# Kernel optimization log

Hardware: AMD Instinct MI355X
Metric: run time of the kernel (lower is better)

## Reference

```python
import jax, jax.numpy as jnp
import numpy as np

N_AGENTS = 12
N_THREADS = 4096
DIM = 3
N_VEC = 4
HID = 64
INV_NF = 32
LAYERS = 2
N = N_THREADS * N_AGENTS


def _intra_graph_edges():
    # fully-connected directed edges within each env's agent graph
    i, j = np.meshgrid(np.arange(N_AGENTS), np.arange(N_AGENTS), indexing='ij')
    mask = i != j
    ri, ci = i[mask], j[mask]  # [132]
    off = (np.arange(N_THREADS) * N_AGENTS)[:, None]
    row = (ri[None, :] + off).reshape(-1).astype(np.int32)
    col = (ci[None, :] + off).reshape(-1).astype(np.int32)
    return jnp.asarray(row), jnp.asarray(col)


def setup_inputs() -> dict:
    key = jax.random.key(0)
    ks = jax.random.split(key, 16)
    s = 0.05
    row, col = _intra_graph_edges()
    return {
        'h0': jax.random.normal(ks[0], (N, INV_NF), jnp.float32),
        'x0': jax.random.normal(ks[1], (N, DIM, N_VEC), jnp.float32),
        'W_embed': jax.random.normal(ks[2], (INV_NF, HID), jnp.float32) * s,
        'b_embed': jnp.zeros((HID,), jnp.float32),
        'We1': jax.random.normal(ks[3], (LAYERS, 2 * HID + N_VEC, HID), jnp.float32) * s,
        'be1': jnp.zeros((LAYERS, HID), jnp.float32),
        'We2': jax.random.normal(ks[4], (LAYERS, HID, HID), jnp.float32) * s,
        'be2': jnp.zeros((LAYERS, HID), jnp.float32),
        'Wx': jax.random.normal(ks[5], (LAYERS, HID, N_VEC), jnp.float32) * s,
        'bx': jnp.zeros((LAYERS, N_VEC), jnp.float32),
        'Wh1': jax.random.normal(ks[6], (LAYERS, 2 * HID, HID), jnp.float32) * s,
        'bh1': jnp.zeros((LAYERS, HID), jnp.float32),
        'Wh2': jax.random.normal(ks[7], (LAYERS, HID, HID), jnp.float32) * s,
        'bh2': jnp.zeros((LAYERS, HID), jnp.float32),
        'w_act': jax.random.normal(ks[8], (N_VEC,), jnp.float32) * s,
        'log_std': jnp.full((DIM,), -0.5, jnp.float32),
        'row': row,
        'col': col,
    }


def reference(h0, x0, W_embed, b_embed, We1, be1, We2, be2, Wx, bx,
              Wh1, bh1, Wh2, bh2, w_act, log_std, row, col):
    silu = jax.nn.silu
    n = h0.shape[0]
    h = h0 @ W_embed + b_embed            # node embedding, [N, HID]
    x = x0                                 # equivariant features, [N, DIM, N_VEC]
    deg = jnp.maximum(jax.ops.segment_sum(jnp.ones_like(row, jnp.float32), row, num_segments=n), 1.0)
    for l in range(LAYERS):
        hi, hj = h[row], h[col]
        diff = x[row] - x[col]                        # [E, DIM, N_VEC]
        radial = jnp.sum(diff * diff, axis=1)          # [E, N_VEC]
        m = silu(jnp.concatenate([hi, hj, radial], -1) @ We1[l] + be1[l])
        m = silu(m @ We2[l] + be2[l])                  # edge messages [E, HID]
        wc = m @ Wx[l] + bx[l]                         # per-vector coord weights [E, N_VEC]
        x = x + jax.ops.segment_sum(diff * wc[:, None, :], row, num_segments=n) / deg[:, None, None]
        agg = jax.ops.segment_sum(m, row, num_segments=n)
        h = h + silu(jnp.concatenate([h, agg], -1) @ Wh1[l] + bh1[l]) @ Wh2[l] + bh2[l]
    mu = jnp.einsum('ndv,v->nd', x, w_act)             # act_net: Linear(N_VEC,1,bias=False)
    actions = mu                                        # deterministic: mode of Normal(mu, std)
    log_probs = jnp.broadcast_to(-log_std - 0.5 * jnp.log(2.0 * jnp.pi), mu.shape)
    actions = actions.reshape(N_THREADS, N_AGENTS, DIM)
    log_probs = log_probs.reshape(N_THREADS, N_AGENTS, DIM)
    return actions, log_probs
```

## Files before the change

### kernel.cpp

```cpp
#include <hip/hip_runtime.h>

#define NAG 12
#define NTH 4096
#define NEDGE 132
#define LDB 72
#define LDT 20

typedef __bf16 bf16_8 __attribute__((ext_vector_type(8)));
typedef __bf16 bf16_4 __attribute__((ext_vector_type(4)));
typedef float  f32x4  __attribute__((ext_vector_type(4)));

#define MFMA(a,b,c) __builtin_amdgcn_mfma_f32_16x16x32_bf16((a),(b),(c),0,0,0)

#define WS_FRAGS 100
#define WS_BIAS_F32 25600
#define WS_BX_F32   27648
#define WS_BYTES 111104

__device__ __forceinline__ float silu_f(float z) {
    float e = __expf(-z);
    return z * __builtin_amdgcn_rcpf(1.0f + e);
}

__device__ __forceinline__ bf16_8 loadB64(const float* __restrict__ W, int kbase, int n, int q) {
    bf16_8 b;
    #pragma unroll
    for (int j = 0; j < 8; ++j) b[j] = (__bf16)W[(kbase + q*8 + j) * 64 + n];
    return b;
}

__device__ __forceinline__ bf16_8 packA8(const float* S) {
    f32x4 u = *(const f32x4*)S, v = *(const f32x4*)(S + 4);
    bf16_8 a;
    a[0]=(__bf16)u.x; a[1]=(__bf16)u.y; a[2]=(__bf16)u.z; a[3]=(__bf16)u.w;
    a[4]=(__bf16)v.x; a[5]=(__bf16)v.y; a[6]=(__bf16)v.z; a[7]=(__bf16)v.w;
    return a;
}

__global__ __launch_bounds__(64) void prep_frags(
    const float* __restrict__ W_embed, const float* __restrict__ We1,
    const float* __restrict__ We2, const float* __restrict__ Wh1,
    const float* __restrict__ Wh2,
    const float* __restrict__ be1, const float* __restrict__ be2,
    const float* __restrict__ bh1, const float* __restrict__ bh2,
    const float* __restrict__ bx, __bf16* __restrict__ wsb)
{
    const int f = blockIdx.x, lane = threadIdx.x;
    const int q = lane >> 4, n16 = lane & 15;
    float* wsf = (float*)wsb;
    if (f < WS_FRAGS) {
        const float* src; int kbase, nbase;
        if (f < 4) { src = W_embed; kbase = 0; nbase = f * 16; }
        else {
            int g0 = f - 4, l = g0 / 48, r = g0 % 48;
            if      (r < 8)  { int nt=r>>1, kh=r&1;            src = We1 + l*NEDGE*64; kbase = kh*32;      nbase = nt*16; }
            else if (r < 16) { int rr=r-8,  nt=rr>>1, kh=rr&1; src = We1 + l*NEDGE*64; kbase = 64 + kh*32; nbase = nt*16; }
            else if (r < 24) { int rr=r-16, nt=rr>>1, kh=rr&1; src = We2 + l*64*64;    kbase = kh*32;      nbase = nt*16; }
            else if (r < 40) { int rr=r-24, nt=rr>>2, ks=rr&3; src = Wh1 + l*128*64;   kbase = ks*32;      nbase = nt*16; }
            else             { int rr=r-40, nt=rr>>1, kh=rr&1; src = Wh2 + l*64*64;    kbase = kh*32;      nbase = nt*16; }
        }
        bf16_8 b = loadB64(src, kbase, nbase + n16, q);
        *(bf16_8*)(wsb + (size_t)f * 512 + lane * 8) = b;
    } else if (f < WS_FRAGS + 8) {
        int f2 = f - WS_FRAGS, l = f2 >> 2, w = f2 & 3;
        const float* src = (w == 0 ? be1 : w == 1 ? be2 : w == 2 ? bh1 : bh2) + l * 64;
        f32x4 v = { src[n16], src[16 + n16], src[32 + n16], src[48 + n16] };
        *(f32x4*)(wsf + WS_BIAS_F32 + ((size_t)(l*4 + w) * 64 + lane) * 4) = v;
    } else {
        #pragma unroll
        for (int l = 0; l < 2; ++l)
            wsf[WS_BX_F32 + l*64 + lane] = (n16 < 4) ? bx[l*4 + n16] : 0.f;
    }
}

template<bool WS>
__device__ __forceinline__ bf16_8 frg(const __bf16* __restrict__ wsb, int fid,
                                      const float* __restrict__ src, int kbase, int n, int lane) {
    if (WS) return *(const bf16_8*)(wsb + (size_t)fid * 512 + lane * 8);
    else    return loadB64(src, kbase, n, (lane >> 4));
}

template<bool WS>
__global__ void __launch_bounds__(64) egnn11(
    const float* __restrict__ h0, const float* __restrict__ x0,
    const float* __restrict__ W_embed, const float* __restrict__ b_embed,
    const float* __restrict__ We1, const float* __restrict__ be1,
    const float* __restrict__ We2, const float* __restrict__ be2,
    const float* __restrict__ Wx, const float* __restrict__ bx,
    const float* __restrict__ Wh1, const float* __restrict__ bh1,
    const float* __restrict__ Wh2, const float* __restrict__ bh2,
    const float* __restrict__ w_act, const float* __restrict__ log_std,
    const __bf16* __restrict__ wsb, float* __restrict__ out)
{
    __shared__ __align__(16) __bf16 sh  [2][NAG * LDB];
    __shared__ __align__(16) __bf16 sHa [2][NAG * LDB];
    __shared__ __align__(16) __bf16 sHb [2][NAG * LDB];
    __shared__ __align__(16) __bf16 mstT[2][2][64 * LDT];
    __shared__ __align__(16) float  sx  [2][NAG * 16];
    __shared__ __align__(16) float  sRad[2][NEDGE * 4];
    __shared__ __align__(16) __bf16 sWcB[2][NEDGE * 4];
    __shared__ __align__(16) float  sWb [4 * 64];

    const int lane = threadIdx.x;
    const int q = lane >> 4, n16 = lane & 15;
    const int rowA = (n16 < NAG) ? n16 : (NAG - 1);
    const int env0 = blockIdx.x * 2;
    const float* wsf = (const float*)wsb;

    if (lane < NAG * 3) {
        int d = lane % 3;
        float lp = -log_std[d] - 0.9189385332046727f;
        out[NTH * NAG * 3 + (env0 + 0) * (NAG*3) + lane] = lp;
        out[NTH * NAG * 3 + (env0 + 1) * (NAG*3) + lane] = lp;
    }

    #pragma unroll
    for (int p = 0; p < 5; ++p) {
        int idx = p * 64 + lane;
        if (idx < 2 * NAG * 12) {
            int ep = idx / 144, r2 = idx - ep * 144;
            sx[ep][(r2 / 12) * 16 + r2 % 12] = x0[(env0) * NAG * 12 + idx];
        }
    }

    f32x4 hC[2][4];
    {
        bf16_8 a[2];
        #pragma unroll
        for (int ep = 0; ep < 2; ++ep)
            a[ep] = packA8(h0 + ((env0 + ep) * NAG + rowA) * 32 + q * 8);
        #pragma unroll
        for (int nt = 0; nt < 4; ++nt) {
            bf16_8 b = frg<WS>(wsb, nt, W_embed, 0, nt*16 + n16, lane);
            float bias = b_embed[nt*16 + n16];
            #pragma unroll
            for (int ep = 0; ep < 2; ++ep) {
                f32x4 acc = {0.f,0.f,0.f,0.f};
                acc = MFMA(a[ep], b, acc);
                #pragma unroll
                for (int r = 0; r < 4; ++r) acc[r] += bias;
                hC[ep][nt] = acc;
            }
        }
        #pragma unroll
        for (int ep = 0; ep < 2; ++ep)
            #pragma unroll
            for (int nt = 0; nt < 4; ++nt)
                #pragma unroll
                for (int r = 0; r < 4; ++r) {
                    int row = q*4 + r;
                    if (row < NAG) sh[ep][row*LDB + nt*16 + n16] = (__bf16)hC[ep][nt][r];
                }
    }

    #pragma unroll 1
    for (int l = 0; l < 2; ++l) {
        const float* We1l = We1 + l * NEDGE * 64;
        const float* be1l = be1 + l * 64;
        const float* be2l = be2 + l * 64;
        const float* Wxl  = Wx  + l * 64 * 4;
        const float* bxl  = bx  + l * 4;
        const float* We2l = We2 + l * 64 * 64;
        const float* Wh1l = Wh1 + l * 128 * 64;
        const float* bh1l = bh1 + l * 64;
        const float* Wh2l = Wh2 + l * 64 * 64;
        const float* bh2l = bh2 + l * 64;
        const int L = 4 + l * 48;

        f32x4 be1q, be2q, bh1q, bh2q;
        float bxv;
        if (WS) {
            const float* bb = wsf + WS_BIAS_F32 + (size_t)(l*4) * 256 + lane * 4;
            be1q = *(const f32x4*)(bb);
            be2q = *(const f32x4*)(bb + 256);
            bh1q = *(const f32x4*)(bb + 512);
            bh2q = *(const f32x4*)(bb + 768);
            bxv  = wsf[WS_BX_F32 + l*64 + lane];
        } else {
            #pragma unroll
            for (int nt = 0; nt < 4; ++nt) {
                be1q[nt] = be1l[nt*16+n16]; be2q[nt] = be2l[nt*16+n16];
                bh1q[nt] = bh1l[nt*16+n16]; bh2q[nt] = bh2l[nt*16+n16];
            }
            bxv = (n16 < 4) ? bxl[n16] : 0.f;
        }

        {
            bf16_8 a0[2], a1[2];
            #pragma unroll
            for (int ep = 0; ep < 2; ++ep) {
                a0[ep] = *(const bf16_8*)(sh[ep] + rowA*LDB + q*8);
                a1[ep] = *(const bf16_8*)(sh[ep] + rowA*LDB + 32 + q*8);
            }
            #pragma unroll
            for (int nt = 0; nt < 4; ++nt) {
                bf16_8 b0 = frg<WS>(wsb, L+nt*2+0,   We1l, 0,  nt*16+n16, lane);
                bf16_8 b1 = frg<WS>(wsb, L+nt*2+1,   We1l, 32, nt*16+n16, lane);
                bf16_8 c0 = frg<WS>(wsb, L+8+nt*2+0, We1l, 64, nt*16+n16, lane);
                bf16_8 c1 = frg<WS>(wsb, L+8+nt*2+1, We1l, 96, nt*16+n16, lane);
                #pragma unroll
                for (int ep = 0; ep < 2; ++ep) {
                    f32x4 aA = {0.f,0.f,0.f,0.f}, aB = {0.f,0.f,0.f,0.f};
                    aA = MFMA(a0[ep], b0, aA); aA = MFMA(a1[ep], b1, aA);
                    aB = MFMA(a0[ep], c0, aB); aB = MFMA(a1[ep], c1, aB);
                    #pragma unroll
                    for (int r = 0; r < 4; ++r) {
                        int row = q*4 + r;
                        if (row < NAG) {
                            sHa[ep][row*LDB + nt*16+n16] = (__bf16)(aA[r] + be1q[nt]);
                            sHb[ep][row*LDB + nt*16+n16] = (__bf16)aB[r];
                        }
                    }
                }
            }
        }
        #pragma unroll
        for (int p = 0; p < 4; ++p) sWb[p*64 + lane] = We1l[(128+p)*64 + lane];
        #pragma unroll
        for (int p = 0; p < 9; ++p) {
            int idx = p * 64 + lane;
            if (idx < NEDGE * 4) {
                int e = idx >> 2, v = idx & 3;
                int i = e / 11, jj = e - i * 11, j = jj + (jj >= i);
                #pragma unroll
                for (int ep = 0; ep < 2; ++ep) {
                    float r = 0.f;
                    #pragma unroll
                    for (int d = 0; d < 3; ++d) {
                        float df = sx[ep][i*16 + d*4 + v] - sx[ep][j*16 + d*4 + v];
                        r += df * df;
                    }
                    sRad[ep][idx] = r;
                }
            }
        }

        float agg[2][NAG];
        #pragma unroll
        for (int ep = 0; ep < 2; ++ep)
            #pragma unroll
            for (int i = 0; i < NAG; ++i) agg[ep][i] = 0.f;
        bf16_8 w2f[4][2], wxf[2];
        #pragma unroll
        for (int nt = 0; nt < 4; ++nt) {
            w2f[nt][0] = frg<WS>(wsb, L+16+nt*2+0, We2l, 0,  nt*16+n16, lane);
            w2f[nt][1] = frg<WS>(wsb, L+16+nt*2+1, We2l, 32, nt*16+n16, lane);
        }
        #pragma unroll
        for (int kh = 0; kh < 2; ++kh) {
            bf16_8 b;
            #pragma unroll
            for (int j2 = 0; j2 < 8; ++j2)
                b[j2] = (n16 < 4) ? (__bf16)Wxl[(kh*32 + q*8 + j2)*4 + n16] : (__bf16)0.f;
            wxf[kh] = b;
        }

        #pragma unroll
        for (int t = 0; t < 9; ++t) {
            const int e  = t*16 + n16;
            const int ec = (e < NEDGE) ? e : (NEDGE - 1);
            const int i  = ec / 11;
            const int jj = ec - i * 11;
            const int j  = jj + (jj >= i);
            bf16_8 af[2][2];
            #pragma unroll
            for (int ep = 0; ep < 2; ++ep) {
                const f32x4 rd = *(const f32x4*)(sRad[ep] + ec * 4);
                #pragma unroll
                for (int kh = 0; kh < 2; ++kh) {
                    const int cb = kh*32 + q*8;
                    bf16_8 ha = *(const bf16_8*)(sHa[ep] + i*LDB + cb);
                    bf16_8 hb = *(const bf16_8*)(sHb[ep] + j*LDB + cb);
                    f32x4 wr0 = {0.f,0.f,0.f,0.f}, wr1 = {0.f,0.f,0.f,0.f};
                    #pragma unroll
                    for (int v = 0; v < 4; ++v) {
                        f32x4 wa = *(const f32x4*)(sWb + v*64 + cb);
                        f32x4 wb = *(const f32x4*)(sWb + v*64 + cb + 4);
                        wr0 += rd[v] * wa; wr1 += rd[v] * wb;
                    }
                    bf16_8 a;
                    #pragma unroll
                    for (int c = 0; c < 4; ++c)
                        a[c]   = (__bf16)silu_f((float)ha[c]   + (float)hb[c]   + wr0[c]);
                    #pragma unroll
                    for (int c = 0; c < 4; ++c)
                        a[4+c] = (__bf16)silu_f((float)ha[4+c] + (float)hb[4+c] + wr1[c]);
                    af[ep][kh] = a;
                }
            }
            #pragma unroll
            for (int ep = 0; ep < 2; ++ep) {
                __bf16* mT = &mstT[ep][t & 1][0];
                #pragma unroll
                for (int nt = 0; nt < 4; ++nt) {
                    f32x4 acc = {0.f,0.f,0.f,0.f};
                    acc = MFMA(af[ep][0], w2f[nt][0], acc);
                    acc = MFMA(af[ep][1], w2f[nt][1], acc);
                    bf16_4 mv;
                    #pragma unroll
                    for (int r = 0; r < 4; ++r) mv[r] = (__bf16)silu_f(acc[r] + be2q[nt]);
                    *(bf16_4*)(mT + (nt*16 + n16)*LDT + q*4) = mv;
                }
            }
            #pragma unroll
            for (int ep = 0; ep < 2; ++ep) {
                const __bf16* mT = &mstT[ep][t & 1][0];
                bf16_8 aw0, aw1;
                #pragma unroll
                for (int j2 = 0; j2 < 8; ++j2) {
                    aw0[j2] = mT[(q*8 + j2)*LDT + n16];
                    aw1[j2] = mT[(32 + q*8 + j2)*LDT + n16];
                }
                f32x4 acc = {0.f,0.f,0.f,0.f};
                acc = MFMA(aw0, wxf[0], acc);
                acc = MFMA(aw1, wxf[1], acc);
                if (n16 < 4) {
                    #pragma unroll
                    for (int r = 0; r < 4; ++r) {
                        int row = t*16 + q*4 + r;
                        if (row < NEDGE) sWcB[ep][row*4 + n16] = (__bf16)(acc[r] + bxv);
                    }
                }
            }
            #pragma unroll
            for (int ep = 0; ep < 2; ++ep) {
                const __bf16* mT = &mstT[ep][t & 1][0];
                bf16_4 c0 = *(const bf16_4*)(mT + lane*LDT + 0);
                #pragma unroll
                for (int el = 0; el < 4; ++el) agg[ep][(t*16 + el)/11] += (float)c0[el];
                if (t < 8) {
                    bf16_4 c1 = *(const bf16_4*)(mT + lane*LDT + 4);
                    bf16_4 c2 = *(const bf16_4*)(mT + lane*LDT + 8);
                    bf16_4 c3 = *(const bf16_4*)(mT + lane*LDT + 12);
                    #pragma unroll
                    for (int el = 0; el < 4; ++el) {
                        agg[ep][(t*16 + 4  + el)/11] += (float)c1[el];
                        agg[ep][(t*16 + 8  + el)/11] += (float)c2[el];
                        agg[ep][(t*16 + 12 + el)/11] += (float)c3[el];
                    }
                }
            }
        }
        #pragma unroll
        for (int ep = 0; ep < 2; ++ep)
            #pragma unroll
            for (int i = 0; i < NAG; ++i) sHb[ep][i*LDB + lane] = (__bf16)agg[ep][i];

        float xn[2][3];
        #pragma unroll
        for (int p = 0; p < 3; ++p) {
            int idx = p*64 + lane;
            int xi = idx / 12, dv = idx % 12, v = dv & 3;
            bool act = idx < 144;
            int xic = act ? xi : 0;
            #pragma unroll
            for (int ep = 0; ep < 2; ++ep) {
                float xiv = sx[ep][xic*16 + dv];
                float acc = 0.f;
                #pragma unroll
                for (int j2 = 0; j2 < NAG; ++j2) {
                    int e2 = xic*11 + j2 - (j2 > xic ? 1 : 0);
                    e2 = (e2 < NEDGE) ? e2 : (NEDGE - 1);
                    float term = (xiv - sx[ep][j2*16 + dv]) * (float)sWcB[ep][e2*4 + v];
                    acc += (j2 == xic) ? 0.f : term;
                }
                xn[ep][p] = act ? (xiv + acc * (1.0f / 11.0f)) : 0.f;
            }
        }
        {
            bf16_8 ah0[2], ah1[2], ag0[2], ag1[2];
            #pragma unroll
            for (int ep = 0; ep < 2; ++ep) {
                ah0[ep] = *(const bf16_8*)(sh[ep]  + rowA*LDB + q*8);
                ah1[ep] = *(const bf16_8*)(sh[ep]  + rowA*LDB + 32 + q*8);
                ag0[ep] = *(const bf16_8*)(sHb[ep] + rowA*LDB + q*8);
                ag1[ep] = *(const bf16_8*)(sHb[ep] + rowA*LDB + 32 + q*8);
            }
            #pragma unroll
            for (int nt = 0; nt < 4; ++nt) {
                bf16_8 b0 = frg<WS>(wsb, L+24+nt*4+0, Wh1l, 0,  nt*16+n16, lane);
                bf16_8 b1 = frg<WS>(wsb, L+24+nt*4+1, Wh1l, 32, nt*16+n16, lane);
                bf16_8 b2 = frg<WS>(wsb, L+24+nt*4+2, Wh1l, 64, nt*16+n16, lane);
                bf16_8 b3 = frg<WS>(wsb, L+24+nt*4+3, Wh1l, 96, nt*16+n16, lane);
                #pragma unroll
                for (int ep = 0; ep < 2; ++ep) {
                    f32x4 acc = {0.f,0.f,0.f,0.f};
                    acc = MFMA(ah0[ep], b0, acc); acc = MFMA(ah1[ep], b1, acc);
                    acc = MFMA(ag0[ep], b2, acc); acc = MFMA(ag1[ep], b3, acc);
                    #pragma unroll
                    for (int r = 0; r < 4; ++r) {
                        int row = q*4 + r;
                        if (row < NAG) sHa[ep][row*LDB + nt*16+n16] = (__bf16)silu_f(acc[r] + bh1q[nt]);
                    }
                }
            }
        }
        #pragma unroll
        for (int p = 0; p < 3; ++p) {
            int idx = p*64 + lane;
            if (idx < 144) {
                #pragma unroll
                for (int ep = 0; ep < 2; ++ep)
                    sx[ep][(idx/12)*16 + idx%12] = xn[ep][p];
            }
        }
        {
            bf16_8 at0[2], at1[2];
            #pragma unroll
            for (int ep = 0; ep < 2; ++ep) {
                at0[ep] = *(const bf16_8*)(sHa[ep] + rowA*LDB + q*8);
                at1[ep] = *(const bf16_8*)(sHa[ep] + rowA*LDB + 32 + q*8);
            }
            #pragma unroll
            for (int nt = 0; nt < 4; ++nt) {
                bf16_8 b0 = frg<WS>(wsb, L+40+nt*2+0, Wh2l, 0,  nt*16+n16, lane);
                bf16_8 b1 = frg<WS>(wsb, L+40+nt*2+1, Wh2l, 32, nt*16+n16, lane);
                #pragma unroll
                for (int ep = 0; ep < 2; ++ep) {
                    f32x4 acc = {0.f,0.f,0.f,0.f};
                    acc = MFMA(at0[ep], b0, acc);
                    acc = MFMA(at1[ep], b1, acc);
                    #pragma unroll
                    for (int r = 0; r < 4; ++r) hC[ep][nt][r] += acc[r] + bh2q[nt];
                }
            }
            #pragma unroll
            for (int ep = 0; ep < 2; ++ep)
                #pragma unroll
                for (int nt = 0; nt < 4; ++nt)
                    #pragma unroll
                    for (int r = 0; r < 4; ++r) {
                        int row = q*4 + r;
                        if (row < NAG) sh[ep][row*LDB + nt*16+n16] = (__bf16)hC[ep][nt][r];
                    }
        }
    }

    if (lane < NAG * 3) {
        int i = lane / 3, d = lane - i * 3;
        #pragma unroll
        for (int ep = 0; ep < 2; ++ep) {
            float mu = 0.f;
            #pragma unroll
            for (int v = 0; v < 4; ++v) mu += sx[ep][i*16 + d*4 + v] * w_act[v];
            out[(env0 + ep) * (NAG*3) + lane] = mu;
        }
    }
}

extern "C" void kernel_launch(void* const* d_in, const int* in_sizes, int n_in,
                              void* d_out, int out_size, void* d_ws, size_t ws_size,
                              hipStream_t stream) {
    const float* h0   = (const float*)d_in[0];
    const float* x0   = (const float*)d_in[1];
    const float* Wem  = (const float*)d_in[2];
    const float* bem  = (const float*)d_in[3];
    const float* We1  = (const float*)d_in[4];
    const float* be1  = (const float*)d_in[5];
    const float* We2  = (const float*)d_in[6];
    const float* be2  = (const float*)d_in[7];
    const float* Wx   = (const float*)d_in[8];
    const float* bx   = (const float*)d_in[9];
    const float* Wh1  = (const float*)d_in[10];
    const float* bh1  = (const float*)d_in[11];
    const float* Wh2  = (const float*)d_in[12];
    const float* bh2  = (const float*)d_in[13];
    const float* wact = (const float*)d_in[14];
    const float* lstd = (const float*)d_in[15];
    float* out = (float*)d_out;

    if (ws_size >= (size_t)WS_BYTES) {
        prep_frags<<<dim3(WS_FRAGS + 9), dim3(64), 0, stream>>>(
            Wem, We1, We2, Wh1, Wh2, be1, be2, bh1, bh2, bx, (__bf16*)d_ws);
        egnn11<true><<<dim3(NTH / 2), dim3(64), 0, stream>>>(
            h0, x0, Wem, bem, We1, be1, We2, be2, Wx, bx,
            Wh1, bh1, Wh2, bh2, wact, lstd, (const __bf16*)d_ws, out);
    } else {
        egnn11<false><<<dim3(NTH / 2), dim3(64), 0, stream>>>(
            h0, x0, Wem, bem, We1, be1, We2, be2, Wx, bx,
            Wh1, bh1, Wh2, bh2, wact, lstd, nullptr, out);
    }
}
```

Measured before the change: 225.7 us.

## Process three environments per wavefront and keep the residual h in LDS

Each 64-thread block now handles three environments instead of two, so each weight fragment loaded from the workspace is reused across more MFMA tiles. The blocks change from 2048 to 1366, and the last block runs a partial tail guarded by nev. To free registers for the larger batch, the fp32 residual hC is removed and the residual update now reads back and rewrites the bf16 h in LDS. This adds a bf16 rounding step to the residual stream, raises LDS use per block, and adds runtime tail checks.

```diff
diff --git a/kernel.cpp b/kernel.cpp
--- a/kernel.cpp
+++ b/kernel.cpp
@@ -5,6 +5,7 @@
 #define NEDGE 132
 #define LDB 72
 #define LDT 20
+#define NE 3
 
 typedef __bf16 bf16_8 __attribute__((ext_vector_type(8)));
 typedef __bf16 bf16_4 __attribute__((ext_vector_type(4)));
@@ -81,7 +82,7 @@
 }
 
 template<bool WS>
-__global__ void __launch_bounds__(64) egnn11(
+__global__ void __launch_bounds__(64) egnn12(
     const float* __restrict__ h0, const float* __restrict__ x0,
     const float* __restrict__ W_embed, const float* __restrict__ b_embed,
     const float* __restrict__ We1, const float* __restrict__ be1,
@@ -92,65 +93,60 @@
     const float* __restrict__ w_act, const float* __restrict__ log_std,
     const __bf16* __restrict__ wsb, float* __restrict__ out)
 {
-    __shared__ __align__(16) __bf16 sh  [2][NAG * LDB];
-    __shared__ __align__(16) __bf16 sHa [2][NAG * LDB];
-    __shared__ __align__(16) __bf16 sHb [2][NAG * LDB];
-    __shared__ __align__(16) __bf16 mstT[2][2][64 * LDT];
-    __shared__ __align__(16) float  sx  [2][NAG * 16];
-    __shared__ __align__(16) float  sRad[2][NEDGE * 4];
-    __shared__ __align__(16) __bf16 sWcB[2][NEDGE * 4];
+    __shared__ __align__(16) __bf16 sh  [NE][NAG * LDB];
+    __shared__ __align__(16) __bf16 sHa [NE][NAG * LDB];
+    __shared__ __align__(16) __bf16 sHb [NE][NAG * LDB];
+    __shared__ __align__(16) __bf16 mstT[NE][2][64 * LDT];
+    __shared__ __align__(16) float  sx  [NE][NAG * 16];
+    __shared__ __align__(16) float  sRad[NE][NEDGE * 4];
+    __shared__ __align__(16) __bf16 sWcB[NE][NEDGE * 4];
     __shared__ __align__(16) float  sWb [4 * 64];
 
     const int lane = threadIdx.x;
     const int q = lane >> 4, n16 = lane & 15;
     const int rowA = (n16 < NAG) ? n16 : (NAG - 1);
-    const int env0 = blockIdx.x * 2;
+    const int env0 = blockIdx.x * NE;
+    const int nev  = (NTH - env0 < NE) ? (NTH - env0) : NE;
     const float* wsf = (const float*)wsb;
 
     if (lane < NAG * 3) {
         int d = lane % 3;
         float lp = -log_std[d] - 0.9189385332046727f;
-        out[NTH * NAG * 3 + (env0 + 0) * (NAG*3) + lane] = lp;
-        out[NTH * NAG * 3 + (env0 + 1) * (NAG*3) + lane] = lp;
+        #pragma unroll
+        for (int ep = 0; ep < NE; ++ep)
+            if (ep < nev) out[NTH * NAG * 3 + (env0 + ep) * (NAG*3) + lane] = lp;
     }
 
     #pragma unroll
-    for (int p = 0; p < 5; ++p) {
+    for (int p = 0; p < 7; ++p) {
         int idx = p * 64 + lane;
-        if (idx < 2 * NAG * 12) {
+        if (idx < nev * 144) {
             int ep = idx / 144, r2 = idx - ep * 144;
-            sx[ep][(r2 / 12) * 16 + r2 % 12] = x0[(env0) * NAG * 12 + idx];
-        }
-    }
-
-    f32x4 hC[2][4];
+            sx[ep][(r2 / 12) * 16 + r2 % 12] = x0[env0 * NAG * 12 + idx];
+        }
+    }
+
     {
-        bf16_8 a[2];
-        #pragma unroll
-        for (int ep = 0; ep < 2; ++ep)
-            a[ep] = packA8(h0 + ((env0 + ep) * NAG + rowA) * 32 + q * 8);
+        bf16_8 a[NE];
+        #pragma unroll
+        for (int ep = 0; ep < NE; ++ep)
+            if (ep < nev) a[ep] = packA8(h0 + ((env0 + ep) * NAG + rowA) * 32 + q * 8);
         #pragma unroll
         for (int nt = 0; nt < 4; ++nt) {
             bf16_8 b = frg<WS>(wsb, nt, W_embed, 0, nt*16 + n16, lane);
             float bias = b_embed[nt*16 + n16];
             #pragma unroll
-            for (int ep = 0; ep < 2; ++ep) {
+            for (int ep = 0; ep < NE; ++ep) {
+                if (ep >= nev) continue;
                 f32x4 acc = {0.f,0.f,0.f,0.f};
                 acc = MFMA(a[ep], b, acc);
                 #pragma unroll
-                for (int r = 0; r < 4; ++r) acc[r] += bias;
-                hC[ep][nt] = acc;
-            }
-        }
-        #pragma unroll
-        for (int ep = 0; ep < 2; ++ep)
-            #pragma unroll
-            for (int nt = 0; nt < 4; ++nt)
-                #pragma unroll
                 for (int r = 0; r < 4; ++r) {
                     int row = q*4 + r;
-                    if (row < NAG) sh[ep][row*LDB + nt*16 + n16] = (__bf16)hC[ep][nt][r];
-                }
+                    if (row < NAG) sh[ep][row*LDB + nt*16 + n16] = (__bf16)(acc[r] + bias);
+                }
+            }
+        }
     }
 
     #pragma unroll 1
@@ -186,9 +182,10 @@
         }
 
         {
-            bf16_8 a0[2], a1[2];
-            #pragma unroll
-            for (int ep = 0; ep < 2; ++ep) {
+            bf16_8 a0[NE], a1[NE];
+            #pragma unroll
+            for (int ep = 0; ep < NE; ++ep) {
+                if (ep >= nev) continue;
                 a0[ep] = *(const bf16_8*)(sh[ep] + rowA*LDB + q*8);
                 a1[ep] = *(const bf16_8*)(sh[ep] + rowA*LDB + 32 + q*8);
             }
@@ -199,7 +196,8 @@
                 bf16_8 c0 = frg<WS>(wsb, L+8+nt*2+0, We1l, 64, nt*16+n16, lane);
                 bf16_8 c1 = frg<WS>(wsb, L+8+nt*2+1, We1l, 96, nt*16+n16, lane);
                 #pragma unroll
-                for (int ep = 0; ep < 2; ++ep) {
+                for (int ep = 0; ep < NE; ++ep) {
+                    if (ep >= nev) continue;
                     f32x4 aA = {0.f,0.f,0.f,0.f}, aB = {0.f,0.f,0.f,0.f};
                     aA = MFMA(a0[ep], b0, aA); aA = MFMA(a1[ep], b1, aA);
                     aB = MFMA(a0[ep], c0, aB); aB = MFMA(a1[ep], c1, aB);
@@ -223,7 +221,8 @@
                 int e = idx >> 2, v = idx & 3;
                 int i = e / 11, jj = e - i * 11, j = jj + (jj >= i);
                 #pragma unroll
-                for (int ep = 0; ep < 2; ++ep) {
+                for (int ep = 0; ep < NE; ++ep) {
+                    if (ep >= nev) continue;
                     float r = 0.f;
                     #pragma unroll
                     for (int d = 0; d < 3; ++d) {
@@ -235,9 +234,9 @@
             }
         }
 
-        float agg[2][NAG];
-        #pragma unroll
-        for (int ep = 0; ep < 2; ++ep)
+        float agg[NE][NAG];
+        #pragma unroll
+        for (int ep = 0; ep < NE; ++ep)
             #pragma unroll
             for (int i = 0; i < NAG; ++i) agg[ep][i] = 0.f;
         bf16_8 w2f[4][2], wxf[2];
@@ -262,9 +261,10 @@
             const int i  = ec / 11;
             const int jj = ec - i * 11;
             const int j  = jj + (jj >= i);
-            bf16_8 af[2][2];
-            #pragma unroll
-            for (int ep = 0; ep < 2; ++ep) {
+            bf16_8 af[NE][2];
+            #pragma unroll
+            for (int ep = 0; ep < NE; ++ep) {
+                if (ep >= nev) continue;
                 const f32x4 rd = *(const f32x4*)(sRad[ep] + ec * 4);
                 #pragma unroll
                 for (int kh = 0; kh < 2; ++kh) {
@@ -289,7 +289,8 @@
                 }
             }
             #pragma unroll
-            for (int ep = 0; ep < 2; ++ep) {
+            for (int ep = 0; ep < NE; ++ep) {
+                if (ep >= nev) continue;
                 __bf16* mT = &mstT[ep][t & 1][0];
                 #pragma unroll
                 for (int nt = 0; nt < 4; ++nt) {
@@ -303,7 +304,8 @@
                 }
             }
             #pragma unroll
-            for (int ep = 0; ep < 2; ++ep) {
+            for (int ep = 0; ep < NE; ++ep) {
+                if (ep >= nev) continue;
                 const __bf16* mT = &mstT[ep][t & 1][0];
                 bf16_8 aw0, aw1;
                 #pragma unroll
@@ -323,7 +325,8 @@
                 }
             }
             #pragma unroll
-            for (int ep = 0; ep < 2; ++ep) {
+            for (int ep = 0; ep < NE; ++ep) {
+                if (ep >= nev) continue;
                 const __bf16* mT = &mstT[ep][t & 1][0];
                 bf16_4 c0 = *(const bf16_4*)(mT + lane*LDT + 0);
                 #pragma unroll
@@ -342,11 +345,13 @@
             }
         }
         #pragma unroll
-        for (int ep = 0; ep < 2; ++ep)
+        for (int ep = 0; ep < NE; ++ep) {
+            if (ep >= nev) continue;
             #pragma unroll
             for (int i = 0; i < NAG; ++i) sHb[ep][i*LDB + lane] = (__bf16)agg[ep][i];
-
-        float xn[2][3];
+        }
+
+        float xn[NE][3];
         #pragma unroll
         for (int p = 0; p < 3; ++p) {
             int idx = p*64 + lane;
@@ -354,7 +359,8 @@
             bool act = idx < 144;
             int xic = act ? xi : 0;
             #pragma unroll
-            for (int ep = 0; ep < 2; ++ep) {
+            for (int ep = 0; ep < NE; ++ep) {
+                if (ep >= nev) continue;
                 float xiv = sx[ep][xic*16 + dv];
                 float acc = 0.f;
                 #pragma unroll
@@ -368,9 +374,10 @@
             }
         }
         {
-            bf16_8 ah0[2], ah1[2], ag0[2], ag1[2];
-            #pragma unroll
-            for (int ep = 0; ep < 2; ++ep) {
+            bf16_8 ah0[NE], ah1[NE], ag0[NE], ag1[NE];
+            #pragma unroll
+            for (int ep = 0; ep < NE; ++ep) {
+                if (ep >= nev) continue;
                 ah0[ep] = *(const bf16_8*)(sh[ep]  + rowA*LDB + q*8);
                 ah1[ep] = *(const bf16_8*)(sh[ep]  + rowA*LDB + 32 + q*8);
                 ag0[ep] = *(const bf16_8*)(sHb[ep] + rowA*LDB + q*8);
@@ -383,7 +390,8 @@
                 bf16_8 b2 = frg<WS>(wsb, L+24+nt*4+2, Wh1l, 64, nt*16+n16, lane);
                 bf16_8 b3 = frg<WS>(wsb, L+24+nt*4+3, Wh1l, 96, nt*16+n16, lane);
                 #pragma unroll
-                for (int ep = 0; ep < 2; ++ep) {
+                for (int ep = 0; ep < NE; ++ep) {
+                    if (ep >= nev) continue;
                     f32x4 acc = {0.f,0.f,0.f,0.f};
                     acc = MFMA(ah0[ep], b0, acc); acc = MFMA(ah1[ep], b1, acc);
                     acc = MFMA(ag0[ep], b2, acc); acc = MFMA(ag1[ep], b3, acc);
@@ -400,14 +408,15 @@
             int idx = p*64 + lane;
             if (idx < 144) {
                 #pragma unroll
-                for (int ep = 0; ep < 2; ++ep)
-                    sx[ep][(idx/12)*16 + idx%12] = xn[ep][p];
+                for (int ep = 0; ep < NE; ++ep)
+                    if (ep < nev) sx[ep][(idx/12)*16 + idx%12] = xn[ep][p];
             }
         }
         {
-            bf16_8 at0[2], at1[2];
-            #pragma unroll
-            for (int ep = 0; ep < 2; ++ep) {
+            bf16_8 at0[NE], at1[NE];
+            #pragma unroll
+            for (int ep = 0; ep < NE; ++ep) {
+                if (ep >= nev) continue;
                 at0[ep] = *(const bf16_8*)(sHa[ep] + rowA*LDB + q*8);
                 at1[ep] = *(const bf16_8*)(sHa[ep] + rowA*LDB + 32 + q*8);
             }
@@ -416,30 +425,29 @@
                 bf16_8 b0 = frg<WS>(wsb, L+40+nt*2+0, Wh2l, 0,  nt*16+n16, lane);
                 bf16_8 b1 = frg<WS>(wsb, L+40+nt*2+1, Wh2l, 32, nt*16+n16, lane);
                 #pragma unroll
-                for (int ep = 0; ep < 2; ++ep) {
+                for (int ep = 0; ep < NE; ++ep) {
+                    if (ep >= nev) continue;
                     f32x4 acc = {0.f,0.f,0.f,0.f};
                     acc = MFMA(at0[ep], b0, acc);
                     acc = MFMA(at1[ep], b1, acc);
                     #pragma unroll
-                    for (int r = 0; r < 4; ++r) hC[ep][nt][r] += acc[r] + bh2q[nt];
-                }
-            }
-            #pragma unroll
-            for (int ep = 0; ep < 2; ++ep)
-                #pragma unroll
-                for (int nt = 0; nt < 4; ++nt)
-                    #pragma unroll
                     for (int r = 0; r < 4; ++r) {
                         int row = q*4 + r;
-                        if (row < NAG) sh[ep][row*LDB + nt*16+n16] = (__bf16)hC[ep][nt][r];
-                    }
+                        if (row < NAG) {
+                            int o = row*LDB + nt*16+n16;
+                            sh[ep][o] = (__bf16)((float)sh[ep][o] + acc[r] + bh2q[nt]);
+                        }
+                    }
+                }
+            }
         }
     }
 
     if (lane < NAG * 3) {
         int i = lane / 3, d = lane - i * 3;
         #pragma unroll
-        for (int ep = 0; ep < 2; ++ep) {
+        for (int ep = 0; ep < NE; ++ep) {
+            if (ep >= nev) continue;
             float mu = 0.f;
             #pragma unroll
             for (int v = 0; v < 4; ++v) mu += sx[ep][i*16 + d*4 + v] * w_act[v];
@@ -468,15 +476,16 @@
     const float* wact = (const float*)d_in[14];
     const float* lstd = (const float*)d_in[15];
     float* out = (float*)d_out;
+    const int nblk = (NTH + NE - 1) / NE;
 
     if (ws_size >= (size_t)WS_BYTES) {
         prep_frags<<<dim3(WS_FRAGS + 9), dim3(64), 0, stream>>>(
             Wem, We1, We2, Wh1, Wh2, be1, be2, bh1, bh2, bx, (__bf16*)d_ws);
-        egnn11<true><<<dim3(NTH / 2), dim3(64), 0, stream>>>(
+        egnn12<true><<<dim3(nblk), dim3(64), 0, stream>>>(
             h0, x0, Wem, bem, We1, be1, We2, be2, Wx, bx,
             Wh1, bh1, Wh2, bh2, wact, lstd, (const __bf16*)d_ws, out);
     } else {
-        egnn11<false><<<dim3(NTH / 2), dim3(64), 0, stream>>>(
+        egnn12<false><<<dim3(nblk), dim3(64), 0, stream>>>(
             h0, x0, Wem, bem, We1, be1, We2, be2, Wx, bx,
             Wh1, bh1, Wh2, bh2, wact, lstd, nullptr, out);
     }
```

Result: slower. 315.4 us (+39.8%).
